# Kernel tuning notes

Measured on AMD Instinct MI355X. Metric: run time of the kernel, lower is better.

Reference implementation:

```python
import jax, jax.numpy as jnp
import numpy as np

B, H, KVH, D = 32, 32, 8, 128
BLOCK_SIZE = 16
MAX_BLOCKS = 256            # per sequence
NUM_BLOCKS = B * MAX_BLOCKS # total cache blocks
MAX_KV = MAX_BLOCKS * BLOCK_SIZE  # 4096
SCALE = 0.08838834764831845       # 1/sqrt(head_dim)


def setup_inputs() -> dict:
    key = jax.random.key(0)
    kq, kk, kv, kkc, kvc, kcl = jax.random.split(key, 6)
    q = jax.random.normal(kq, (B, H, D), dtype=jnp.float32)
    k = jax.random.normal(kk, (B, KVH, D), dtype=jnp.float32)
    v = jax.random.normal(kv, (B, KVH, D), dtype=jnp.float32)
    k_cache = jax.random.normal(kkc, (NUM_BLOCKS, BLOCK_SIZE, KVH, D), dtype=jnp.float32)
    v_cache = jax.random.normal(kvc, (NUM_BLOCKS, BLOCK_SIZE, KVH, D), dtype=jnp.float32)
    # each sequence owns a disjoint contiguous range of cache blocks
    block_tables = jnp.arange(NUM_BLOCKS, dtype=jnp.int32).reshape(B, MAX_BLOCKS)
    context_lens = jax.random.randint(kcl, (B,), 1, MAX_KV + 1).astype(jnp.int32)
    # new token is stored at logical position context_len - 1 of each sequence
    last = context_lens - 1
    blk = jnp.take_along_axis(block_tables, (last // BLOCK_SIZE)[:, None], axis=1)[:, 0]
    slot_mapping = (blk.astype(jnp.int64) * BLOCK_SIZE + (last % BLOCK_SIZE).astype(jnp.int64))
    return {
        "q": q, "k": k, "v": v,
        "k_cache": k_cache, "v_cache": v_cache,
        "block_tables": block_tables,
        "context_lens": context_lens,
        "slot_mapping": slot_mapping,
    }


def reference(q, k, v, k_cache, v_cache, block_tables, context_lens, slot_mapping):
    # --- store_kvcache: write new k/v tokens into the paged cache ---
    blk = slot_mapping // BLOCK_SIZE
    off = slot_mapping % BLOCK_SIZE
    k_cache = k_cache.at[blk, off].set(k)
    v_cache = v_cache.at[blk, off].set(v)

    # --- paged gather: [B, MAX_BLOCKS, BS, KVH, D] -> [B, MAX_KV, KVH, D] ---
    k_seq = k_cache[block_tables].reshape(B, MAX_KV, KVH, D)
    v_seq = v_cache[block_tables].reshape(B, MAX_KV, KVH, D)

    # --- GQA decode attention (one query token per sequence) ---
    g = H // KVH  # queries per kv head
    qg = q.reshape(B, KVH, g, D)
    scores = jnp.einsum("bkgd,bskd->bkgs", qg, k_seq) * SCALE  # [B,KVH,g,MAX_KV]
    valid = jnp.arange(MAX_KV, dtype=jnp.int32)[None, :] < context_lens[:, None]
    scores = jnp.where(valid[:, None, None, :], scores, -jnp.inf)
    w = jax.nn.softmax(scores.astype(jnp.float32), axis=-1).astype(q.dtype)
    o = jnp.einsum("bkgs,bskd->bkgd", w, v_seq).reshape(B, H, D)
    return o
```

## Files before the change

kernel.cpp:

```cpp
#include <hip/hip_runtime.h>
#include <math.h>

#define BB      32
#define KVH     8
#define GQ      4
#define HD      128
#define BS      16
#define MAXBLK  256
#define CHUNK   256
#define NCHUNK  16
#define NUNIT   8
#define IUN     2
#define SWEEP   (NUNIT * IUN)

#define QSCALE  (0.08838834764831845f * 1.4426950408889634f)

__global__ __launch_bounds__(256)
void attn_partial(const float* __restrict__ q,
                  const float* __restrict__ knew,
                  const float* __restrict__ vnew,
                  const float* __restrict__ kc,
                  const float* __restrict__ vc,
                  const int*   __restrict__ btab,
                  const int*   __restrict__ ctxlen,
                  float* __restrict__ part_o,
                  float* __restrict__ part_l)
{
    const int bk    = blockIdx.x;
    const int chunk = blockIdx.y;
    const int b     = bk / KVH;
    const int kvh   = bk % KVH;

    const int ctx = ctxlen[b];
    const int s0  = chunk * CHUNK;
    if (s0 >= ctx) return;
    const int s_end = min(s0 + CHUNK, ctx);
    const int last  = ctx - 1;

    const int tid = threadIdx.x;
    const int u   = tid >> 5;
    const int ln  = tid & 31;
    const int d4  = ln * 4;
    const int h   = ln & 3;
    const bool odd = (ln & 1) != 0;
    const bool hi  = (ln & 2) != 0;

    __shared__ int   s_bt[CHUNK / BS];
    __shared__ float s_l[NUNIT][GQ];
    __shared__ float s_acc[NUNIT][GQ][HD];

    if (tid < CHUNK / BS)
        s_bt[tid] = btab[b * MAXBLK + (s0 >> 4) + tid];

    float4 qv[GQ];
#pragma unroll
    for (int g = 0; g < GQ; ++g) {
        const float* qp = q + ((size_t)(b * (KVH * GQ) + kvh * GQ + g)) * HD + d4;
        float4 t = *(const float4*)qp;
        qv[g] = make_float4(t.x * QSCALE, t.y * QSCALE, t.z * QSCALE, t.w * QSCALE);
    }

    float  l[GQ];
    float4 acc[GQ];
#pragma unroll
    for (int j = 0; j < GQ; ++j) {
        l[j] = 0.f;
        acc[j] = make_float4(0.f, 0.f, 0.f, 0.f);
    }

    const float* knew_row = knew + (size_t)(b * KVH + kvh) * HD;
    const float* vnew_row = vnew + (size_t)(b * KVH + kvh) * HD;

    __syncthreads();

    const int niter = (s_end - s0 + SWEEP - 1) / SWEEP;

    auto load2 = [&](int j, float4& k0, float4& k1, float4& v0, float4& v1) {
        const int sbase = s0 + j * SWEEP + u * IUN;
#pragma unroll
        for (int i = 0; i < IUN; ++i) {
            int s = sbase + i;
            int sc_ = min(s, s_end - 1);
            const int pb = s_bt[(sc_ - s0) >> 4];
            const long long roff =
                ((long long)pb * BS + (sc_ & (BS - 1))) * (KVH * HD) + kvh * HD;
            const bool isnew = (sc_ == last);
            const float* kr = isnew ? knew_row : (kc + roff);
            const float* vr = isnew ? vnew_row : (vc + roff);
            float4 kf = *(const float4*)(kr + d4);
            float4 vf = *(const float4*)(vr + d4);
            if (i == 0) { k0 = kf; v0 = vf; } else { k1 = kf; v1 = vf; }
        }
    };

    auto proc2 = [&](int j, const float4& k0, const float4& k1,
                     const float4& v0, const float4& v1) {
        const int sbase = s0 + j * SWEEP + u * IUN;
        const bool val0 = (sbase     < s_end);
        const bool val1 = (sbase + 1 < s_end);

        float e0[GQ], e1[GQ];
#pragma unroll
        for (int g = 0; g < GQ; ++g) {
            e0[g] = qv[g].x * k0.x + qv[g].y * k0.y + qv[g].z * k0.z + qv[g].w * k0.w;
            e1[g] = qv[g].x * k1.x + qv[g].y * k1.y + qv[g].z * k1.z + qv[g].w * k1.w;
        }

        float A0 = (odd ? e0[1] : e0[0]) + __shfl_xor(odd ? e0[0] : e0[1], 1);
        float B0 = (odd ? e0[3] : e0[2]) + __shfl_xor(odd ? e0[2] : e0[3], 1);
        float A1 = (odd ? e1[1] : e1[0]) + __shfl_xor(odd ? e1[0] : e1[1], 1);
        float B1 = (odd ? e1[3] : e1[2]) + __shfl_xor(odd ? e1[2] : e1[3], 1);
        float r0 = (hi ? B0 : A0) + __shfl_xor(hi ? A0 : B0, 2);
        float r1 = (hi ? B1 : A1) + __shfl_xor(hi ? A1 : B1, 2);
        r0 += __shfl_xor(r0, 4);  r1 += __shfl_xor(r1, 4);
        r0 += __shfl_xor(r0, 8);  r1 += __shfl_xor(r1, 8);
        r0 += __shfl_xor(r0, 16); r1 += __shfl_xor(r1, 16);

        const float p0 = val0 ? exp2f(r0) : 0.f;
        const float p1 = val1 ? exp2f(r1) : 0.f;

        float pa0[GQ], pa1[GQ];
        pa0[0] = p0;                 pa1[0] = p1;
        pa0[1] = __shfl_xor(p0, 1);  pa1[1] = __shfl_xor(p1, 1);
        pa0[2] = __shfl_xor(p0, 2);  pa1[2] = __shfl_xor(p1, 2);
        pa0[3] = __shfl_xor(p0, 3);  pa1[3] = __shfl_xor(p1, 3);

#pragma unroll
        for (int jj = 0; jj < GQ; ++jj) {
            l[jj] += pa0[jj] + pa1[jj];
            acc[jj].x += pa0[jj] * v0.x + pa1[jj] * v1.x;
            acc[jj].y += pa0[jj] * v0.y + pa1[jj] * v1.y;
            acc[jj].z += pa0[jj] * v0.z + pa1[jj] * v1.z;
            acc[jj].w += pa0[jj] * v0.w + pa1[jj] * v1.w;
        }
    };

    float4 kA0, kA1, vA0, vA1, kB0, kB1, vB0, vB1;
    load2(0, kA0, kA1, vA0, vA1);
    int j = 0;
    while (true) {
        if (j + 1 < niter) load2(j + 1, kB0, kB1, vB0, vB1);
        proc2(j, kA0, kA1, vA0, vA1);
        ++j; if (j >= niter) break;
        if (j + 1 < niter) load2(j + 1, kA0, kA1, vA0, vA1);
        proc2(j, kB0, kB1, vB0, vB1);
        ++j; if (j >= niter) break;
    }

#pragma unroll
    for (int jj = 0; jj < GQ; ++jj)
        *(float4*)&s_acc[u][h ^ jj][d4] = acc[jj];
    if (ln == 0) {
#pragma unroll
        for (int jj = 0; jj < GQ; ++jj) s_l[u][jj] = l[jj];
    }
    __syncthreads();

    if (tid < HD) {
        const int d = tid;
        const long long ebase = (long long)bk * NCHUNK + chunk;
#pragma unroll
        for (int g = 0; g < GQ; ++g) {
            float L = 0.f, O = 0.f;
#pragma unroll
            for (int uu = 0; uu < NUNIT; ++uu) {
                L += s_l[uu][g];
                O += s_acc[uu][g][d];
            }
            part_o[(ebase * GQ + g) * HD + d] = O;
            if (d == 0) part_l[ebase * GQ + g] = L;
        }
    }
}

__global__ __launch_bounds__(128)
void attn_reduce(const float* __restrict__ part_o,
                 const float* __restrict__ part_l,
                 const int*   __restrict__ ctxlen,
                 float* __restrict__ out)
{
    const int bk  = blockIdx.x;
    const int b   = bk / KVH;
    const int kvh = bk % KVH;
    const int d   = threadIdx.x;

    const int ctx = ctxlen[b];
    const int nc  = (ctx + CHUNK - 1) / CHUNK;
    const long long ebase = (long long)bk * NCHUNK;

#pragma unroll
    for (int g = 0; g < GQ; ++g) {
        float L = 0.f, O = 0.f;
        for (int c = 0; c < nc; ++c) {
            L += part_l[(ebase + c) * GQ + g];
            O += part_o[((ebase + c) * GQ + g) * HD + d];
        }
        out[((size_t)(b * (KVH * GQ) + kvh * GQ + g)) * HD + d] = O / L;
    }
}

extern "C" void kernel_launch(void* const* d_in, const int* in_sizes, int n_in,
                              void* d_out, int out_size, void* d_ws, size_t ws_size,
                              hipStream_t stream)
{
    const float* q  = (const float*)d_in[0];
    const float* k  = (const float*)d_in[1];
    const float* v  = (const float*)d_in[2];
    const float* kc = (const float*)d_in[3];
    const float* vc = (const float*)d_in[4];
    const int*   bt = (const int*)d_in[5];
    const int*   cl = (const int*)d_in[6];

    float* out = (float*)d_out;

    float* part_o = (float*)d_ws;
    float* part_l = part_o + (size_t)BB * KVH * NCHUNK * GQ * HD;

    dim3 g1(BB * KVH, NCHUNK);
    attn_partial<<<g1, 256, 0, stream>>>(q, k, v, kc, vc, bt, cl,
                                         part_o, part_l);
    attn_reduce<<<dim3(BB * KVH), 128, 0, stream>>>(part_o, part_l, cl, out);
}
```

Measured before the change: 121.4 us.

## Use 16-lane units with 8 elements per lane and shuffle-reduce across units

Each key position is now handled by 16 lanes holding 8 head-dim elements each, so a block runs 16 units instead of 8 and covers twice as many positions per sweep. The dot-product reduction needs fewer shuffle stages, and the per-unit accumulators are first reduced across the units inside a wavefront with shuffles before shared memory is used, which shrinks the shared buffer to four rows. The cost is more registers per thread (wider q, K/V and accumulator sets), partly offset by a launch-bounds occupancy hint of three blocks. It also adds extra shuffles for broadcasting the softmax weights.

Measured after the change: 147.6 us. 21.6% more time.

```diff
diff --git a/kernel.cpp b/kernel.cpp
--- a/kernel.cpp
+++ b/kernel.cpp
@@ -9,13 +9,14 @@
 #define MAXBLK  256
 #define CHUNK   256
 #define NCHUNK  16
-#define NUNIT   8
+#define UN      16
+#define NUNIT   16
 #define IUN     2
 #define SWEEP   (NUNIT * IUN)
 
 #define QSCALE  (0.08838834764831845f * 1.4426950408889634f)
 
-__global__ __launch_bounds__(256)
+__global__ __launch_bounds__(256, 3)
 void attn_partial(const float* __restrict__ q,
                   const float* __restrict__ knew,
                   const float* __restrict__ vnew,
@@ -38,34 +39,38 @@
     const int last  = ctx - 1;
 
     const int tid = threadIdx.x;
-    const int u   = tid >> 5;
-    const int ln  = tid & 31;
-    const int d4  = ln * 4;
-    const int h   = ln & 3;
-    const bool odd = (ln & 1) != 0;
-    const bool hi  = (ln & 2) != 0;
+    const int u   = tid >> 4;
+    const int lu  = tid & 15;
+    const int d8  = lu * 8;
+    const bool lb1 = (lu & 1) != 0;
+    const bool lb2 = (lu & 2) != 0;
+    const bool lb4 = (lu & 4) != 0;
+    const int mypos = (lu >> 2) & 1;
 
     __shared__ int   s_bt[CHUNK / BS];
-    __shared__ float s_l[NUNIT][GQ];
-    __shared__ float s_acc[NUNIT][GQ][HD];
+    __shared__ float s_l[4][GQ];
+    __shared__ float s_acc[4][GQ][HD];
 
     if (tid < CHUNK / BS)
         s_bt[tid] = btab[b * MAXBLK + (s0 >> 4) + tid];
 
-    float4 qv[GQ];
+    float4 qa[GQ], qb[GQ];
 #pragma unroll
     for (int g = 0; g < GQ; ++g) {
-        const float* qp = q + ((size_t)(b * (KVH * GQ) + kvh * GQ + g)) * HD + d4;
-        float4 t = *(const float4*)qp;
-        qv[g] = make_float4(t.x * QSCALE, t.y * QSCALE, t.z * QSCALE, t.w * QSCALE);
+        const float* qp = q + ((size_t)(b * (KVH * GQ) + kvh * GQ + g)) * HD + d8;
+        float4 ta = *(const float4*)(qp);
+        float4 tb = *(const float4*)(qp + 4);
+        qa[g] = make_float4(ta.x * QSCALE, ta.y * QSCALE, ta.z * QSCALE, ta.w * QSCALE);
+        qb[g] = make_float4(tb.x * QSCALE, tb.y * QSCALE, tb.z * QSCALE, tb.w * QSCALE);
     }
 
     float  l[GQ];
-    float4 acc[GQ];
+    float4 acca[GQ], accb[GQ];
 #pragma unroll
     for (int j = 0; j < GQ; ++j) {
         l[j] = 0.f;
-        acc[j] = make_float4(0.f, 0.f, 0.f, 0.f);
+        acca[j] = make_float4(0.f, 0.f, 0.f, 0.f);
+        accb[j] = make_float4(0.f, 0.f, 0.f, 0.f);
     }
 
     const float* knew_row = knew + (size_t)(b * KVH + kvh) * HD;
@@ -75,84 +80,121 @@
 
     const int niter = (s_end - s0 + SWEEP - 1) / SWEEP;
 
-    auto load2 = [&](int j, float4& k0, float4& k1, float4& v0, float4& v1) {
+    auto loadpos = [&](int s, float4& ka, float4& kb, float4& va, float4& vb) {
+        const int sc_ = min(s, s_end - 1);
+        const int pb = s_bt[(sc_ - s0) >> 4];
+        const long long roff =
+            ((long long)pb * BS + (sc_ & (BS - 1))) * (KVH * HD) + kvh * HD;
+        const bool isnew = (sc_ == last);
+        const float* kr = isnew ? knew_row : (kc + roff);
+        const float* vr = isnew ? vnew_row : (vc + roff);
+        ka = *(const float4*)(kr + d8);
+        kb = *(const float4*)(kr + d8 + 4);
+        va = *(const float4*)(vr + d8);
+        vb = *(const float4*)(vr + d8 + 4);
+    };
+    auto load2 = [&](int j, float4& k0a, float4& k0b, float4& k1a, float4& k1b,
+                            float4& v0a, float4& v0b, float4& v1a, float4& v1b) {
         const int sbase = s0 + j * SWEEP + u * IUN;
-#pragma unroll
-        for (int i = 0; i < IUN; ++i) {
-            int s = sbase + i;
-            int sc_ = min(s, s_end - 1);
-            const int pb = s_bt[(sc_ - s0) >> 4];
-            const long long roff =
-                ((long long)pb * BS + (sc_ & (BS - 1))) * (KVH * HD) + kvh * HD;
-            const bool isnew = (sc_ == last);
-            const float* kr = isnew ? knew_row : (kc + roff);
-            const float* vr = isnew ? vnew_row : (vc + roff);
-            float4 kf = *(const float4*)(kr + d4);
-            float4 vf = *(const float4*)(vr + d4);
-            if (i == 0) { k0 = kf; v0 = vf; } else { k1 = kf; v1 = vf; }
-        }
+        loadpos(sbase,     k0a, k0b, v0a, v0b);
+        loadpos(sbase + 1, k1a, k1b, v1a, v1b);
     };
 
-    auto proc2 = [&](int j, const float4& k0, const float4& k1,
-                     const float4& v0, const float4& v1) {
+#define DOT8(QA, QB, KA, KB) \
+    ((QA).x*(KA).x + (QA).y*(KA).y + (QA).z*(KA).z + (QA).w*(KA).w + \
+     (QB).x*(KB).x + (QB).y*(KB).y + (QB).z*(KB).z + (QB).w*(KB).w)
+
+    auto proc2 = [&](int j, const float4& k0a, const float4& k0b,
+                            const float4& k1a, const float4& k1b,
+                            const float4& v0a, const float4& v0b,
+                            const float4& v1a, const float4& v1b) {
         const int sbase = s0 + j * SWEEP + u * IUN;
-        const bool val0 = (sbase     < s_end);
-        const bool val1 = (sbase + 1 < s_end);
-
-        float e0[GQ], e1[GQ];
-#pragma unroll
-        for (int g = 0; g < GQ; ++g) {
-            e0[g] = qv[g].x * k0.x + qv[g].y * k0.y + qv[g].z * k0.z + qv[g].w * k0.w;
-            e1[g] = qv[g].x * k1.x + qv[g].y * k1.y + qv[g].z * k1.z + qv[g].w * k1.w;
-        }
-
-        float A0 = (odd ? e0[1] : e0[0]) + __shfl_xor(odd ? e0[0] : e0[1], 1);
-        float B0 = (odd ? e0[3] : e0[2]) + __shfl_xor(odd ? e0[2] : e0[3], 1);
-        float A1 = (odd ? e1[1] : e1[0]) + __shfl_xor(odd ? e1[0] : e1[1], 1);
-        float B1 = (odd ? e1[3] : e1[2]) + __shfl_xor(odd ? e1[2] : e1[3], 1);
-        float r0 = (hi ? B0 : A0) + __shfl_xor(hi ? A0 : B0, 2);
-        float r1 = (hi ? B1 : A1) + __shfl_xor(hi ? A1 : B1, 2);
-        r0 += __shfl_xor(r0, 4);  r1 += __shfl_xor(r1, 4);
-        r0 += __shfl_xor(r0, 8);  r1 += __shfl_xor(r1, 8);
-        r0 += __shfl_xor(r0, 16); r1 += __shfl_xor(r1, 16);
-
-        const float p0 = val0 ? exp2f(r0) : 0.f;
-        const float p1 = val1 ? exp2f(r1) : 0.f;
-
-        float pa0[GQ], pa1[GQ];
-        pa0[0] = p0;                 pa1[0] = p1;
-        pa0[1] = __shfl_xor(p0, 1);  pa1[1] = __shfl_xor(p1, 1);
-        pa0[2] = __shfl_xor(p0, 2);  pa1[2] = __shfl_xor(p1, 2);
-        pa0[3] = __shfl_xor(p0, 3);  pa1[3] = __shfl_xor(p1, 3);
-
-#pragma unroll
-        for (int jj = 0; jj < GQ; ++jj) {
-            l[jj] += pa0[jj] + pa1[jj];
-            acc[jj].x += pa0[jj] * v0.x + pa1[jj] * v1.x;
-            acc[jj].y += pa0[jj] * v0.y + pa1[jj] * v1.y;
-            acc[jj].z += pa0[jj] * v0.z + pa1[jj] * v1.z;
-            acc[jj].w += pa0[jj] * v0.w + pa1[jj] * v1.w;
-        }
+
+        float e0 = DOT8(qa[0], qb[0], k0a, k0b);
+        float e1 = DOT8(qa[1], qb[1], k0a, k0b);
+        float e2 = DOT8(qa[2], qb[2], k0a, k0b);
+        float e3 = DOT8(qa[3], qb[3], k0a, k0b);
+        float e4 = DOT8(qa[0], qb[0], k1a, k1b);
+        float e5 = DOT8(qa[1], qb[1], k1a, k1b);
+        float e6 = DOT8(qa[2], qb[2], k1a, k1b);
+        float e7 = DOT8(qa[3], qb[3], k1a, k1b);
+
+        float t0 = (lb1 ? e1 : e0) + __shfl_xor(lb1 ? e0 : e1, 1);
+        float t1 = (lb1 ? e3 : e2) + __shfl_xor(lb1 ? e2 : e3, 1);
+        float t2 = (lb1 ? e5 : e4) + __shfl_xor(lb1 ? e4 : e5, 1);
+        float t3 = (lb1 ? e7 : e6) + __shfl_xor(lb1 ? e6 : e7, 1);
+        float u0 = (lb2 ? t1 : t0) + __shfl_xor(lb2 ? t0 : t1, 2);
+        float u1 = (lb2 ? t3 : t2) + __shfl_xor(lb2 ? t2 : t3, 2);
+        float r  = (lb4 ? u1 : u0) + __shfl_xor(lb4 ? u0 : u1, 4);
+        r += __shfl_xor(r, 8);
+
+        const bool valid = (sbase + mypos) < s_end;
+        const float pp = valid ? exp2f(r) : 0.f;
+
+        float g1 = __shfl_xor(pp, 1);
+        float g2 = __shfl_xor(pp, 2);
+        float g3 = __shfl_xor(g1, 2);
+        float g4 = __shfl_xor(pp, 4);
+        float g5 = __shfl_xor(g1, 4);
+        float g6 = __shfl_xor(g2, 4);
+        float g7 = __shfl_xor(g3, 4);
+
+        const float w0A = lb4 ? g4 : pp;  const float w0B = lb4 ? pp : g4;
+        const float w1A = lb4 ? g5 : g1;  const float w1B = lb4 ? g1 : g5;
+        const float w2A = lb4 ? g6 : g2;  const float w2B = lb4 ? g2 : g6;
+        const float w3A = lb4 ? g7 : g3;  const float w3B = lb4 ? g3 : g7;
+
+        l[0] += w0A + w0B;  l[1] += w1A + w1B;
+        l[2] += w2A + w2B;  l[3] += w3A + w3B;
+
+#define ACC4(AC, WA, WB, VA0, VA1) \
+        (AC).x += (WA)*(VA0).x + (WB)*(VA1).x; \
+        (AC).y += (WA)*(VA0).y + (WB)*(VA1).y; \
+        (AC).z += (WA)*(VA0).z + (WB)*(VA1).z; \
+        (AC).w += (WA)*(VA0).w + (WB)*(VA1).w;
+
+        ACC4(acca[0], w0A, w0B, v0a, v1a)  ACC4(accb[0], w0A, w0B, v0b, v1b)
+        ACC4(acca[1], w1A, w1B, v0a, v1a)  ACC4(accb[1], w1A, w1B, v0b, v1b)
+        ACC4(acca[2], w2A, w2B, v0a, v1a)  ACC4(accb[2], w2A, w2B, v0b, v1b)
+        ACC4(acca[3], w3A, w3B, v0a, v1a)  ACC4(accb[3], w3A, w3B, v0b, v1b)
+#undef ACC4
     };
 
-    float4 kA0, kA1, vA0, vA1, kB0, kB1, vB0, vB1;
-    load2(0, kA0, kA1, vA0, vA1);
+    float4 kA0a,kA0b,kA1a,kA1b,vA0a,vA0b,vA1a,vA1b;
+    float4 kB0a,kB0b,kB1a,kB1b,vB0a,vB0b,vB1a,vB1b;
+    load2(0, kA0a,kA0b,kA1a,kA1b,vA0a,vA0b,vA1a,vA1b);
     int j = 0;
     while (true) {
-        if (j + 1 < niter) load2(j + 1, kB0, kB1, vB0, vB1);
-        proc2(j, kA0, kA1, vA0, vA1);
+        if (j + 1 < niter) load2(j + 1, kB0a,kB0b,kB1a,kB1b,vB0a,vB0b,vB1a,vB1b);
+        proc2(j, kA0a,kA0b,kA1a,kA1b,vA0a,vA0b,vA1a,vA1b);
         ++j; if (j >= niter) break;
-        if (j + 1 < niter) load2(j + 1, kA0, kA1, vA0, vA1);
-        proc2(j, kB0, kB1, vB0, vB1);
+        if (j + 1 < niter) load2(j + 1, kA0a,kA0b,kA1a,kA1b,vA0a,vA0b,vA1a,vA1b);
+        proc2(j, kB0a,kB0b,kB1a,kB1b,vB0a,vB0b,vB1a,vB1b);
         ++j; if (j >= niter) break;
     }
 
-#pragma unroll
-    for (int jj = 0; jj < GQ; ++jj)
-        *(float4*)&s_acc[u][h ^ jj][d4] = acc[jj];
-    if (ln == 0) {
-#pragma unroll
-        for (int jj = 0; jj < GQ; ++jj) s_l[u][jj] = l[jj];
+#define RED2(X) { X += __shfl_xor(X, 16); X += __shfl_xor(X, 32); }
+#pragma unroll
+    for (int jj = 0; jj < GQ; ++jj) {
+        RED2(acca[jj].x) RED2(acca[jj].y) RED2(acca[jj].z) RED2(acca[jj].w)
+        RED2(accb[jj].x) RED2(accb[jj].y) RED2(accb[jj].z) RED2(accb[jj].w)
+        RED2(l[jj])
+    }
+#undef RED2
+
+    const int w    = tid >> 6;
+    const int wlan = tid & 63;
+    if (wlan < UN) {
+#pragma unroll
+        for (int jj = 0; jj < GQ; ++jj) {
+            const int head = (lu & 3) ^ jj;
+            *(float4*)&s_acc[w][head][d8]     = acca[jj];
+            *(float4*)&s_acc[w][head][d8 + 4] = accb[jj];
+        }
+    }
+    if (wlan == 0) {
+#pragma unroll
+        for (int jj = 0; jj < GQ; ++jj) s_l[w][jj] = l[jj];
     }
     __syncthreads();
 
@@ -163,9 +205,9 @@
         for (int g = 0; g < GQ; ++g) {
             float L = 0.f, O = 0.f;
 #pragma unroll
-            for (int uu = 0; uu < NUNIT; ++uu) {
-                L += s_l[uu][g];
-                O += s_acc[uu][g][d];
+            for (int ww = 0; ww < 4; ++ww) {
+                L += s_l[ww][g];
+                O += s_acc[ww][g][d];
             }
             part_o[(ebase * GQ + g) * HD + d] = O;
             if (d == 0) part_l[ebase * GQ + g] = L;
```

## Assign one KV head per warp, reading full contiguous token rows per block

Applied to the files above, without the earlier changes.

Each block now covers one sequence and one 128-token chunk across all 8 KV heads, with each 32-lane group handling one head. Every token row (all heads, 4KB) is read in one contiguous 256-thread sweep, replacing the old layout where eight warps split positions for a single head. This removes the shared-memory cross-unit reduction and its barrier, and partials are written straight to global memory. In exchange each warp walks its chunk serially, so there is less latency hiding per block and twice as many chunks go to the reduce kernel.

After: 160.5 us. 32.2% more time.

```diff
diff --git a/kernel.cpp b/kernel.cpp
--- a/kernel.cpp
+++ b/kernel.cpp
@@ -7,11 +7,8 @@
 #define HD      128
 #define BS      16
 #define MAXBLK  256
-#define CHUNK   256
-#define NCHUNK  16
-#define NUNIT   8
-#define IUN     2
-#define SWEEP   (NUNIT * IUN)
+#define CHUNK   128
+#define NCHUNK  32
 
 #define QSCALE  (0.08838834764831845f * 1.4426950408889634f)
 
@@ -26,10 +23,8 @@
                   float* __restrict__ part_o,
                   float* __restrict__ part_l)
 {
-    const int bk    = blockIdx.x;
+    const int b     = blockIdx.x;
     const int chunk = blockIdx.y;
-    const int b     = bk / KVH;
-    const int kvh   = bk % KVH;
 
     const int ctx = ctxlen[b];
     const int s0  = chunk * CHUNK;
@@ -38,16 +33,14 @@
     const int last  = ctx - 1;
 
     const int tid = threadIdx.x;
-    const int u   = tid >> 5;
+    const int kvh = tid >> 5;
     const int ln  = tid & 31;
     const int d4  = ln * 4;
     const int h   = ln & 3;
     const bool odd = (ln & 1) != 0;
     const bool hi  = (ln & 2) != 0;
 
-    __shared__ int   s_bt[CHUNK / BS];
-    __shared__ float s_l[NUNIT][GQ];
-    __shared__ float s_acc[NUNIT][GQ][HD];
+    __shared__ int s_bt[CHUNK / BS];
 
     if (tid < CHUNK / BS)
         s_bt[tid] = btab[b * MAXBLK + (s0 >> 4) + tid];
@@ -68,35 +61,34 @@
         acc[j] = make_float4(0.f, 0.f, 0.f, 0.f);
     }
 
-    const float* knew_row = knew + (size_t)(b * KVH + kvh) * HD;
-    const float* vnew_row = vnew + (size_t)(b * KVH + kvh) * HD;
+    const float* knew_base = knew + (size_t)b * KVH * HD;
+    const float* vnew_base = vnew + (size_t)b * KVH * HD;
 
     __syncthreads();
 
-    const int niter = (s_end - s0 + SWEEP - 1) / SWEEP;
-
+    const int npos  = s_end - s0;
+    const int niter = (npos + 1) >> 1;
+
+    auto loadpos = [&](int s, float4& kf, float4& vf) {
+        const int sc_ = min(s, s_end - 1);
+        const int pb = s_bt[(sc_ - s0) >> 4];
+        const long long roff =
+            ((long long)pb * BS + (sc_ & (BS - 1))) * (KVH * HD);
+        const bool isnew = (sc_ == last);
+        const float* kr = isnew ? knew_base : (kc + roff);
+        const float* vr = isnew ? vnew_base : (vc + roff);
+        kf = *(const float4*)(kr + tid * 4);
+        vf = *(const float4*)(vr + tid * 4);
+    };
     auto load2 = [&](int j, float4& k0, float4& k1, float4& v0, float4& v1) {
-        const int sbase = s0 + j * SWEEP + u * IUN;
-#pragma unroll
-        for (int i = 0; i < IUN; ++i) {
-            int s = sbase + i;
-            int sc_ = min(s, s_end - 1);
-            const int pb = s_bt[(sc_ - s0) >> 4];
-            const long long roff =
-                ((long long)pb * BS + (sc_ & (BS - 1))) * (KVH * HD) + kvh * HD;
-            const bool isnew = (sc_ == last);
-            const float* kr = isnew ? knew_row : (kc + roff);
-            const float* vr = isnew ? vnew_row : (vc + roff);
-            float4 kf = *(const float4*)(kr + d4);
-            float4 vf = *(const float4*)(vr + d4);
-            if (i == 0) { k0 = kf; v0 = vf; } else { k1 = kf; v1 = vf; }
-        }
+        const int s = s0 + 2 * j;
+        loadpos(s,     k0, v0);
+        loadpos(s + 1, k1, v1);
     };
 
     auto proc2 = [&](int j, const float4& k0, const float4& k1,
                      const float4& v0, const float4& v1) {
-        const int sbase = s0 + j * SWEEP + u * IUN;
-        const bool val0 = (sbase     < s_end);
+        const int sbase = s0 + 2 * j;
         const bool val1 = (sbase + 1 < s_end);
 
         float e0[GQ], e1[GQ];
@@ -116,7 +108,7 @@
         r0 += __shfl_xor(r0, 8);  r1 += __shfl_xor(r1, 8);
         r0 += __shfl_xor(r0, 16); r1 += __shfl_xor(r1, 16);
 
-        const float p0 = val0 ? exp2f(r0) : 0.f;
+        const float p0 = exp2f(r0);
         const float p1 = val1 ? exp2f(r1) : 0.f;
 
         float pa0[GQ], pa1[GQ];
@@ -147,29 +139,15 @@
         ++j; if (j >= niter) break;
     }
 
-#pragma unroll
-    for (int jj = 0; jj < GQ; ++jj)
-        *(float4*)&s_acc[u][h ^ jj][d4] = acc[jj];
+    const long long ebase = (long long)(b * KVH + kvh) * NCHUNK + chunk;
+#pragma unroll
+    for (int jj = 0; jj < GQ; ++jj) {
+        const int head = h ^ jj;
+        *(float4*)&part_o[(ebase * GQ + head) * HD + d4] = acc[jj];
+    }
     if (ln == 0) {
 #pragma unroll
-        for (int jj = 0; jj < GQ; ++jj) s_l[u][jj] = l[jj];
-    }
-    __syncthreads();
-
-    if (tid < HD) {
-        const int d = tid;
-        const long long ebase = (long long)bk * NCHUNK + chunk;
-#pragma unroll
-        for (int g = 0; g < GQ; ++g) {
-            float L = 0.f, O = 0.f;
-#pragma unroll
-            for (int uu = 0; uu < NUNIT; ++uu) {
-                L += s_l[uu][g];
-                O += s_acc[uu][g][d];
-            }
-            part_o[(ebase * GQ + g) * HD + d] = O;
-            if (d == 0) part_l[ebase * GQ + g] = L;
-        }
+        for (int jj = 0; jj < GQ; ++jj) part_l[ebase * GQ + jj] = l[jj];
     }
 }
 
@@ -216,7 +194,7 @@
     float* part_o = (float*)d_ws;
     float* part_l = part_o + (size_t)BB * KVH * NCHUNK * GQ * HD;
 
-    dim3 g1(BB * KVH, NCHUNK);
+    dim3 g1(BB, NCHUNK);
     attn_partial<<<g1, 256, 0, stream>>>(q, k, v, kc, vc, bt, cl,
                                          part_o, part_l);
     attn_reduce<<<dim3(BB * KVH), 128, 0, stream>>>(part_o, part_l, cl, out);
```

## Halve chunk size, specialize last-token path, parallelize reduce over query groups

Applied to the files above, without the earlier changes.

Shrinks the KV chunk from 256 to 128 tokens, doubling the grid of partial-attention blocks so more workgroups can pull cache bandwidth at once. The per-row new-token check is moved into a template specialization that only the chunk containing the last position runs, and the two rows of each pair now share one block-table lookup. The reduce kernel uses 512 threads so each thread handles one (group, dim) pair instead of looping over the four groups. Smaller chunks double the partial-result traffic and the number of items the reduce must sum, and blocks doing little work spend proportionally more time on setup.

Result: faster. 115.0 us (-5.3%).

```diff
diff --git a/kernel.cpp b/kernel.cpp
--- a/kernel.cpp
+++ b/kernel.cpp
@@ -7,13 +7,16 @@
 #define HD      128
 #define BS      16
 #define MAXBLK  256
-#define CHUNK   256
-#define NCHUNK  16
+#define CHUNK   128
+#define CHLOG   7
+#define NCHUNK  32
 #define NUNIT   8
 #define IUN     2
 #define SWEEP   (NUNIT * IUN)
 
 #define QSCALE  (0.08838834764831845f * 1.4426950408889634f)
+
+template <bool B> struct BoolC { static constexpr bool value = B; };
 
 __global__ __launch_bounds__(256)
 void attn_partial(const float* __restrict__ q,
@@ -32,7 +35,7 @@
     const int kvh   = bk % KVH;
 
     const int ctx = ctxlen[b];
-    const int s0  = chunk * CHUNK;
+    const int s0  = chunk << CHLOG;
     if (s0 >= ctx) return;
     const int s_end = min(s0 + CHUNK, ctx);
     const int last  = ctx - 1;
@@ -74,24 +77,6 @@
     __syncthreads();
 
     const int niter = (s_end - s0 + SWEEP - 1) / SWEEP;
-
-    auto load2 = [&](int j, float4& k0, float4& k1, float4& v0, float4& v1) {
-        const int sbase = s0 + j * SWEEP + u * IUN;
-#pragma unroll
-        for (int i = 0; i < IUN; ++i) {
-            int s = sbase + i;
-            int sc_ = min(s, s_end - 1);
-            const int pb = s_bt[(sc_ - s0) >> 4];
-            const long long roff =
-                ((long long)pb * BS + (sc_ & (BS - 1))) * (KVH * HD) + kvh * HD;
-            const bool isnew = (sc_ == last);
-            const float* kr = isnew ? knew_row : (kc + roff);
-            const float* vr = isnew ? vnew_row : (vc + roff);
-            float4 kf = *(const float4*)(kr + d4);
-            float4 vf = *(const float4*)(vr + d4);
-            if (i == 0) { k0 = kf; v0 = vf; } else { k1 = kf; v1 = vf; }
-        }
-    };
 
     auto proc2 = [&](int j, const float4& k0, const float4& k1,
                      const float4& v0, const float4& v1) {
@@ -135,17 +120,47 @@
         }
     };
 
-    float4 kA0, kA1, vA0, vA1, kB0, kB1, vB0, vB1;
-    load2(0, kA0, kA1, vA0, vA1);
-    int j = 0;
-    while (true) {
-        if (j + 1 < niter) load2(j + 1, kB0, kB1, vB0, vB1);
-        proc2(j, kA0, kA1, vA0, vA1);
-        ++j; if (j >= niter) break;
-        if (j + 1 < niter) load2(j + 1, kA0, kA1, vA0, vA1);
-        proc2(j, kB0, kB1, vB0, vB1);
-        ++j; if (j >= niter) break;
-    }
+    auto mainloop = [&](auto haslast_c) {
+        constexpr bool HASLAST = decltype(haslast_c)::value;
+
+        auto load2 = [&](int j, float4& k0, float4& k1, float4& v0, float4& v1) {
+            const int sbase = s0 + j * SWEEP + u * IUN;
+            const int se1   = s_end - 1;
+            const int sc0   = min(sbase, se1);
+            const int sc1   = min(sbase + 1, se1);
+            const int pb    = s_bt[(sc0 - s0) >> 4];
+            const long long roff0 =
+                ((long long)pb * BS + (sc0 & (BS - 1))) * (KVH * HD) + kvh * HD;
+            const long long roff1 = roff0 + (long long)(sc1 - sc0) * (KVH * HD);
+            const float* kr0 = kc + roff0;
+            const float* vr0 = vc + roff0;
+            const float* kr1 = kc + roff1;
+            const float* vr1 = vc + roff1;
+            if (HASLAST) {
+                if (sc0 == last) { kr0 = knew_row; vr0 = vnew_row; }
+                if (sc1 == last) { kr1 = knew_row; vr1 = vnew_row; }
+            }
+            k0 = *(const float4*)(kr0 + d4);
+            v0 = *(const float4*)(vr0 + d4);
+            k1 = *(const float4*)(kr1 + d4);
+            v1 = *(const float4*)(vr1 + d4);
+        };
+
+        float4 kA0, kA1, vA0, vA1, kB0, kB1, vB0, vB1;
+        load2(0, kA0, kA1, vA0, vA1);
+        int j = 0;
+        while (true) {
+            if (j + 1 < niter) load2(j + 1, kB0, kB1, vB0, vB1);
+            proc2(j, kA0, kA1, vA0, vA1);
+            ++j; if (j >= niter) break;
+            if (j + 1 < niter) load2(j + 1, kA0, kA1, vA0, vA1);
+            proc2(j, kB0, kB1, vB0, vB1);
+            ++j; if (j >= niter) break;
+        }
+    };
+
+    if (chunk == (last >> CHLOG)) mainloop(BoolC<true>{});
+    else                          mainloop(BoolC<false>{});
 
 #pragma unroll
     for (int jj = 0; jj < GQ; ++jj)
@@ -173,7 +188,7 @@
     }
 }
 
-__global__ __launch_bounds__(128)
+__global__ __launch_bounds__(512)
 void attn_reduce(const float* __restrict__ part_o,
                  const float* __restrict__ part_l,
                  const int*   __restrict__ ctxlen,
@@ -182,21 +197,19 @@
     const int bk  = blockIdx.x;
     const int b   = bk / KVH;
     const int kvh = bk % KVH;
-    const int d   = threadIdx.x;
+    const int g   = threadIdx.x >> 7;
+    const int d   = threadIdx.x & (HD - 1);
 
     const int ctx = ctxlen[b];
-    const int nc  = (ctx + CHUNK - 1) / CHUNK;
+    const int nc  = (ctx + CHUNK - 1) >> CHLOG;
     const long long ebase = (long long)bk * NCHUNK;
 
-#pragma unroll
-    for (int g = 0; g < GQ; ++g) {
-        float L = 0.f, O = 0.f;
-        for (int c = 0; c < nc; ++c) {
-            L += part_l[(ebase + c) * GQ + g];
-            O += part_o[((ebase + c) * GQ + g) * HD + d];
-        }
-        out[((size_t)(b * (KVH * GQ) + kvh * GQ + g)) * HD + d] = O / L;
-    }
+    float L = 0.f, O = 0.f;
+    for (int c = 0; c < nc; ++c) {
+        L += part_l[(ebase + c) * GQ + g];
+        O += part_o[((ebase + c) * GQ + g) * HD + d];
+    }
+    out[((size_t)(b * (KVH * GQ) + kvh * GQ + g)) * HD + d] = O / L;
 }
 
 extern "C" void kernel_launch(void* const* d_in, const int* in_sizes, int n_in,
@@ -219,5 +232,5 @@
     dim3 g1(BB * KVH, NCHUNK);
     attn_partial<<<g1, 256, 0, stream>>>(q, k, v, kc, vc, bt, cl,
                                          part_o, part_l);
-    attn_reduce<<<dim3(BB * KVH), 128, 0, stream>>>(part_o, part_l, cl, out);
+    attn_reduce<<<dim3(BB * KVH), 512, 0, stream>>>(part_o, part_l, cl, out);
 }
```
